# Performance work log

Measured on AMD Instinct MI355X. Metric: run time of the kernel, lower is better.

Reference implementation:

```python
import jax, jax.numpy as jnp
import numpy as np
import math

D_MODEL = 512
N_HEADS = 8
WINDOW = 32
B, L, S = 4, 2048, 2048


def setup_inputs() -> dict:
    key = jax.random.key(0)
    ks = jax.random.split(key, 12)
    scale = 1.0 / math.sqrt(D_MODEL)
    inp = {
        "queries": jax.random.normal(ks[0], (B, L, D_MODEL), jnp.float32),
        "keys": jax.random.normal(ks[1], (B, S, D_MODEL), jnp.float32),
        "values": jax.random.normal(ks[2], (B, S, D_MODEL), jnp.float32),
        # TriangularCausalMask: True above the diagonal => masked
        "attn_mask": jnp.triu(jnp.ones((L, S), jnp.bool_), k=1)[None, None],
        "Wq": jax.random.normal(ks[3], (D_MODEL, D_MODEL), jnp.float32) * scale,
        "bq": jnp.zeros((D_MODEL,), jnp.float32),
        "Wk": jax.random.normal(ks[4], (D_MODEL, D_MODEL), jnp.float32) * scale,
        "bk": jnp.zeros((D_MODEL,), jnp.float32),
        "Wv": jax.random.normal(ks[5], (D_MODEL, D_MODEL), jnp.float32) * scale,
        "bv": jnp.zeros((D_MODEL,), jnp.float32),
        "Wo": jax.random.normal(ks[6], (D_MODEL, D_MODEL), jnp.float32) * scale,
        "bo": jnp.zeros((D_MODEL,), jnp.float32),
        "gamma": jnp.ones((1,), jnp.float32) * 0.5,
    }
    return inp


def reference(queries, keys, values, attn_mask, Wq, bq, Wk, bk, Wv, bv, Wo, bo, gamma):
    Bq, Lq, _ = queries.shape
    Sq = keys.shape[1]
    H = N_HEADS
    q = (queries @ Wq + bq).reshape(Bq, Lq, H, -1)  # [B,L,H,dk]
    k = (keys @ Wk + bk).reshape(Bq, Sq, H, -1)
    v = (values @ Wv + bv).reshape(Bq, Sq, H, -1)

    scores = jnp.einsum('blhd,bshd->bhls', q, k) / math.sqrt(D_MODEL)  # [B,H,L,S]

    # exponential decay on relative position
    rel = jnp.arange(Lq)[:, None] - jnp.arange(Sq)[None, :]  # [L,S]
    decay = jnp.exp(-gamma[0] * jnp.abs(rel).astype(scores.dtype))
    scores = scores * decay[None, None]

    # sliding-window mask (exact replica of _create_window_mask)
    t = jnp.arange(Lq)
    start = jnp.clip(t - WINDOW // 2, 0, None)
    end = jnp.clip(t + WINDOW // 2 + 1, None, Sq)
    wmask = (t[:, None] >= start[None, :]) & (t[:, None] < end[None, :])  # [L,S]
    neg_inf = jnp.asarray(-jnp.inf, scores.dtype)
    scores = jnp.where(wmask[None, None], scores, neg_inf)

    # causal mask: True = masked
    scores = jnp.where(attn_mask, neg_inf, scores)

    attn = jax.nn.softmax(scores, axis=-1)  # dropout is identity at eval
    context = jnp.einsum('bhls,bshd->blhd', attn, v).reshape(Bq, Lq, -1)
    out = context @ Wo + bo
    return (out, attn)
```

## Files before the change

kernel.cpp:

```cpp
#include <hip/hip_runtime.h>
#include <hip/hip_bf16.h>
#include <cstdint>
#include <cstddef>

#define D_MODEL 512
#define N_HEADS 8
#define HDIM 64
#define SEQ 2048
#define B_SZ 4
#define M_TOT (B_SZ * SEQ)
#define ATTN_ROWS (B_SZ * N_HEADS * SEQ)
#define PROJ_ELEMS ((size_t)M_TOT * D_MODEL)

typedef __bf16 bf16x8 __attribute__((ext_vector_type(8)));
typedef float  f32x4  __attribute__((ext_vector_type(4)));

__device__ __forceinline__ unsigned short f2bf(float x) {
    __bf16 b = (__bf16)x;
    return __builtin_bit_cast(unsigned short, b);
}
__device__ __forceinline__ float bf2f(unsigned short u) {
    __bf16 b = __builtin_bit_cast(__bf16, u);
    return (float)b;
}

__global__ __launch_bounds__(256) void fill_zero(float4* __restrict__ p, size_t n4) {
    size_t i = (size_t)blockIdx.x * blockDim.x + threadIdx.x;
    size_t stride = (size_t)gridDim.x * blockDim.x;
    float4 z; z.x = 0.f; z.y = 0.f; z.z = 0.f; z.w = 0.f;
    for (; i < n4; i += stride) p[i] = z;
}

struct CvtArgs {
    const float* src[3];
    unsigned short* dst[3];
};

__global__ __launch_bounds__(256) void cvt_k(CvtArgs ca) {
    const int z = blockIdx.z;
    const size_t i = ((size_t)blockIdx.x * 256 + threadIdx.x) * 8;
    const float* src = ca.src[z];
    float4 a = *(const float4*)&src[i];
    float4 b = *(const float4*)&src[i + 4];
    unsigned short outv[8];
    outv[0] = f2bf(a.x); outv[1] = f2bf(a.y); outv[2] = f2bf(a.z); outv[3] = f2bf(a.w);
    outv[4] = f2bf(b.x); outv[5] = f2bf(b.y); outv[6] = f2bf(b.z); outv[7] = f2bf(b.w);
    *(uint4*)&ca.dst[z][i] = *(const uint4*)outv;
}

struct TransArgs {
    const float* W[4];
    unsigned short* Wt[4];
};

__global__ void transpose_k(TransArgs ta) {
    __shared__ float tile[32][33];
    const int z = blockIdx.z;
    const float* W = ta.W[z];
    unsigned short* Wt = ta.Wt[z];
    int x = blockIdx.x * 32 + threadIdx.x;
    int y0 = blockIdx.y * 32;
    for (int j = threadIdx.y; j < 32; j += 8)
        tile[j][threadIdx.x] = W[(size_t)(y0 + j) * D_MODEL + x];
    __syncthreads();
    int xo = blockIdx.y * 32 + threadIdx.x;
    int yo0 = blockIdx.x * 32;
    for (int j = threadIdx.y; j < 32; j += 8)
        Wt[(size_t)(yo0 + j) * D_MODEL + xo] = f2bf(tile[threadIdx.x][j]);
}

struct GemmArgs {
    const unsigned short* A[3];
    const unsigned short* Wt[3];
    const float* bias[3];
    void* C[3];
};

#define LDSTRIDE 72

template <int F32OUT>
__global__ __launch_bounds__(256, 2) void gemm_bt(GemmArgs ga) {
    __shared__ __align__(16) unsigned short lsA[128 * LDSTRIDE];
    __shared__ __align__(16) unsigned short lsB[128 * LDSTRIDE];

    const int z = blockIdx.z;
    const unsigned short* __restrict__ A  = ga.A[z];
    const unsigned short* __restrict__ Wt = ga.Wt[z];
    const float* __restrict__ bias        = ga.bias[z];

    const int m0 = blockIdx.x * 128;
    const int n0 = blockIdx.y * 128;
    const int tid = threadIdx.x;
    const int lane = tid & 63;
    const int wid = tid >> 6;
    const int wm = (wid >> 1) * 64;
    const int wn = (wid & 1) * 64;
    const int lrow = lane & 15;
    const int quad = lane >> 4;

    f32x4 acc[4][4];
#pragma unroll
    for (int i = 0; i < 4; ++i)
#pragma unroll
        for (int j = 0; j < 4; ++j)
            acc[i][j] = (f32x4){0.f, 0.f, 0.f, 0.f};

    for (int kt = 0; kt < D_MODEL; kt += 64) {
        __syncthreads();
#pragma unroll
        for (int p = 0; p < 4; ++p) {
            int c = p * 256 + tid;
            int r = c >> 3;
            int col = (c & 7) << 3;
            *(uint4*)&lsA[r * LDSTRIDE + col] =
                *(const uint4*)&A[(size_t)(m0 + r) * D_MODEL + kt + col];
        }
#pragma unroll
        for (int p = 0; p < 4; ++p) {
            int c = p * 256 + tid;
            int r = c >> 3;
            int col = (c & 7) << 3;
            *(uint4*)&lsB[r * LDSTRIDE + col] =
                *(const uint4*)&Wt[(size_t)(n0 + r) * D_MODEL + kt + col];
        }
        __syncthreads();
#pragma unroll
        for (int ks = 0; ks < 2; ++ks) {
            const int ko = ks * 32 + quad * 8;
            bf16x8 af[4], bfr[4];
#pragma unroll
            for (int mt = 0; mt < 4; ++mt)
                af[mt] = *(const bf16x8*)&lsA[(wm + mt * 16 + lrow) * LDSTRIDE + ko];
#pragma unroll
            for (int nt = 0; nt < 4; ++nt)
                bfr[nt] = *(const bf16x8*)&lsB[(wn + nt * 16 + lrow) * LDSTRIDE + ko];
#pragma unroll
            for (int mt = 0; mt < 4; ++mt)
#pragma unroll
                for (int nt = 0; nt < 4; ++nt)
                    acc[mt][nt] = __builtin_amdgcn_mfma_f32_16x16x32_bf16(
                        af[mt], bfr[nt], acc[mt][nt], 0, 0, 0);
        }
    }

#pragma unroll
    for (int nt = 0; nt < 4; ++nt) {
        const int gcol = n0 + wn + nt * 16 + lrow;
        const float bv = bias[gcol];
#pragma unroll
        for (int mt = 0; mt < 4; ++mt) {
            const int grow = m0 + wm + mt * 16 + quad * 4;
#pragma unroll
            for (int r = 0; r < 4; ++r) {
                const float v = acc[mt][nt][r] + bv;
                if (F32OUT)
                    ((float*)ga.C[z])[(size_t)(grow + r) * D_MODEL + gcol] = v;
                else
                    ((unsigned short*)ga.C[z])[(size_t)(grow + r) * D_MODEL + gcol] = f2bf(v);
            }
        }
    }
}

__global__ __launch_bounds__(256, 4) void attn_k(
    const unsigned short* __restrict__ Q,
    const unsigned short* __restrict__ K,
    const unsigned short* __restrict__ V,
    const float* __restrict__ gamma_p,
    float* __restrict__ attn_out,
    unsigned short* __restrict__ ctx) {
    const int wid = threadIdx.x >> 6;
    const int lane = threadIdx.x & 63;
    const int idx = blockIdx.x * 4 + wid;
    const int t = idx & (SEQ - 1);
    const int bh = idx >> 11;
    const int h = bh & (N_HEADS - 1);
    const int b = bh >> 3;

    const float g = gamma_p[0];
    int s0 = t - 16;
    if (s0 < 0) s0 = 0;
    const int cnt = t - s0 + 1;

    const size_t qrow = (size_t)b * SEQ + t;
    const int qcol = h * HDIM + lane;
    const float q = bf2f(Q[qrow * D_MODEL + qcol]);
    const float rs = 0.044194173824159216f;
    const size_t krowbase = (size_t)b * SEQ;

    float myscore = -__builtin_inff();
    float m = -__builtin_inff();
    for (int j = 0; j < cnt; ++j) {
        const int s = s0 + j;
        const float kv = bf2f(K[(krowbase + s) * D_MODEL + qcol]);
        float part = q * kv;
#pragma unroll
        for (int off = 32; off > 0; off >>= 1)
            part += __shfl_xor(part, off, 64);
        const float score = part * rs * __expf(-g * (float)(t - s));
        if (lane == j) myscore = score;
        m = fmaxf(m, score);
    }

    const float p = (lane < cnt) ? __expf(myscore - m) : 0.f;
    float l = p;
#pragma unroll
    for (int off = 32; off > 0; off >>= 1)
        l += __shfl_xor(l, off, 64);
    const float inv = 1.f / l;

    if (lane < cnt)
        attn_out[(size_t)idx * SEQ + s0 + lane] = p * inv;

    float acc = 0.f;
    for (int j = 0; j < cnt; ++j) {
        const float pj = __shfl(p, j, 64) * inv;
        const float vv = bf2f(V[(krowbase + s0 + j) * D_MODEL + qcol]);
        acc = fmaf(pj, vv, acc);
    }
    ctx[qrow * D_MODEL + qcol] = f2bf(acc);
}

extern "C" void kernel_launch(void* const* d_in, const int* in_sizes, int n_in,
                              void* d_out, int out_size, void* d_ws, size_t ws_size,
                              hipStream_t stream) {
    const float* queries = (const float*)d_in[0];
    const float* keys    = (const float*)d_in[1];
    const float* values  = (const float*)d_in[2];
    const float* Wq = (const float*)d_in[4];
    const float* bq = (const float*)d_in[5];
    const float* Wk = (const float*)d_in[6];
    const float* bk = (const float*)d_in[7];
    const float* Wv = (const float*)d_in[8];
    const float* bv = (const float*)d_in[9];
    const float* Wo = (const float*)d_in[10];
    const float* bo = (const float*)d_in[11];
    const float* gamma = (const float*)d_in[12];

    char* ws = (char*)d_ws;
    unsigned short* Qin = (unsigned short*)ws;
    unsigned short* Kin = Qin + PROJ_ELEMS;
    unsigned short* Vin = Kin + PROJ_ELEMS;
    unsigned short* WT  = Vin + PROJ_ELEMS;
    unsigned short* WqT = WT;
    unsigned short* WkT = WT + 262144;
    unsigned short* WvT = WT + 2 * 262144;
    unsigned short* WoT = WT + 3 * 262144;
    unsigned short* Qp  = WT + 4 * 262144;
    unsigned short* Kp  = Qp + PROJ_ELEMS;
    unsigned short* Vp  = Kp + PROJ_ELEMS;
    unsigned short* Ctx = Vp + PROJ_ELEMS;

    float* out_p  = (float*)d_out;
    float* attn_p = out_p + PROJ_ELEMS;

    const size_t n4 = (size_t)ATTN_ROWS * SEQ / 4;
    fill_zero<<<8192, 256, 0, stream>>>((float4*)attn_p, n4);

    CvtArgs ca;
    ca.src[0] = queries; ca.src[1] = keys; ca.src[2] = values;
    ca.dst[0] = Qin;     ca.dst[1] = Kin;  ca.dst[2] = Vin;
    cvt_k<<<dim3(PROJ_ELEMS / (256 * 8), 1, 3), 256, 0, stream>>>(ca);

    TransArgs ta;
    ta.W[0] = Wq;  ta.W[1] = Wk;  ta.W[2] = Wv;  ta.W[3] = Wo;
    ta.Wt[0] = WqT; ta.Wt[1] = WkT; ta.Wt[2] = WvT; ta.Wt[3] = WoT;
    transpose_k<<<dim3(16, 16, 4), dim3(32, 8), 0, stream>>>(ta);

    GemmArgs gq;
    gq.A[0] = Qin;   gq.A[1] = Kin;  gq.A[2] = Vin;
    gq.Wt[0] = WqT;  gq.Wt[1] = WkT; gq.Wt[2] = WvT;
    gq.bias[0] = bq; gq.bias[1] = bk; gq.bias[2] = bv;
    gq.C[0] = Qp;    gq.C[1] = Kp;   gq.C[2] = Vp;
    gemm_bt<0><<<dim3(M_TOT / 128, D_MODEL / 128, 3), 256, 0, stream>>>(gq);

    attn_k<<<ATTN_ROWS / 4, 256, 0, stream>>>(Qp, Kp, Vp, gamma, attn_p, Ctx);

    GemmArgs go;
    go.A[0] = Ctx;   go.Wt[0] = WoT; go.bias[0] = bo; go.C[0] = out_p;
    go.A[1] = Ctx;   go.Wt[1] = WoT; go.bias[1] = bo; go.C[1] = out_p;
    go.A[2] = Ctx;   go.Wt[2] = WoT; go.bias[2] = bo; go.C[2] = out_p;
    gemm_bt<1><<<dim3(M_TOT / 128, D_MODEL / 128, 1), 256, 0, stream>>>(go);
}
```

Before: 766.9 us.

## Tile sliding-window attention with LDS-staged K/V and 4 lanes per query row

Replaces the one-wavefront-per-row attention kernel with a block that handles 64 query rows of one head. The block stages the shared K/V window rows in LDS, and each row is computed by 4 lanes holding 16 dims each. This removes the long serial per-key loop of 64-lane shuffle reductions and the redundant global K/V reads. In exchange it adds LDS usage and register pressure, and makes the attention-probability stores strided across lanes.

```diff
diff --git a/kernel.cpp b/kernel.cpp
--- a/kernel.cpp
+++ b/kernel.cpp
@@ -162,63 +162,107 @@
     }
 }
 
-__global__ __launch_bounds__(256, 4) void attn_k(
+#define KV_ROWS 80
+#define LROW 72
+
+__device__ __forceinline__ void load16f(const unsigned short* p, float* out) {
+    bf16x8 a = *(const bf16x8*)p;
+    bf16x8 b = *(const bf16x8*)(p + 8);
+#pragma unroll
+    for (int i = 0; i < 8; ++i) { out[i] = (float)a[i]; out[8 + i] = (float)b[i]; }
+}
+
+__global__ __launch_bounds__(256, 4) void attn2_k(
     const unsigned short* __restrict__ Q,
     const unsigned short* __restrict__ K,
     const unsigned short* __restrict__ V,
     const float* __restrict__ gamma_p,
     float* __restrict__ attn_out,
     unsigned short* __restrict__ ctx) {
-    const int wid = threadIdx.x >> 6;
-    const int lane = threadIdx.x & 63;
-    const int idx = blockIdx.x * 4 + wid;
-    const int t = idx & (SEQ - 1);
-    const int bh = idx >> 11;
-    const int h = bh & (N_HEADS - 1);
+    __shared__ __align__(16) unsigned short lk[KV_ROWS * LROW];
+    __shared__ __align__(16) unsigned short lv[KV_ROWS * LROW];
+
+    const int bh = blockIdx.y;
+    const int t0 = blockIdx.x * 64;
     const int b = bh >> 3;
+    const int h = bh & 7;
+    const int tid = threadIdx.x;
+    const int w = tid >> 6;
+    const int lane = tid & 63;
+    const int r = lane >> 2;
+    const int c = lane & 3;
 
     const float g = gamma_p[0];
-    int s0 = t - 16;
-    if (s0 < 0) s0 = 0;
-    const int cnt = t - s0 + 1;
-
-    const size_t qrow = (size_t)b * SEQ + t;
-    const int qcol = h * HDIM + lane;
-    const float q = bf2f(Q[qrow * D_MODEL + qcol]);
     const float rs = 0.044194173824159216f;
-    const size_t krowbase = (size_t)b * SEQ;
-
-    float myscore = -__builtin_inff();
-    float m = -__builtin_inff();
-    for (int j = 0; j < cnt; ++j) {
-        const int s = s0 + j;
-        const float kv = bf2f(K[(krowbase + s) * D_MODEL + qcol]);
-        float part = q * kv;
-#pragma unroll
-        for (int off = 32; off > 0; off >>= 1)
-            part += __shfl_xor(part, off, 64);
-        const float score = part * rs * __expf(-g * (float)(t - s));
-        if (lane == j) myscore = score;
-        m = fmaxf(m, score);
-    }
-
-    const float p = (lane < cnt) ? __expf(myscore - m) : 0.f;
-    float l = p;
-#pragma unroll
-    for (int off = 32; off > 0; off >>= 1)
-        l += __shfl_xor(l, off, 64);
+
+    const size_t srcbase = (size_t)b * SEQ * D_MODEL + (size_t)h * HDIM;
+    for (int idx = tid; idx < KV_ROWS * 8; idx += 256) {
+        const int row = idx >> 3;
+        const int ch = (idx & 7) * 8;
+        const int grow = t0 - 16 + row;
+        uint4 kv4 = {0, 0, 0, 0};
+        uint4 vv4 = {0, 0, 0, 0};
+        if (grow >= 0) {
+            const size_t off = srcbase + (size_t)grow * D_MODEL + ch;
+            kv4 = *(const uint4*)&K[off];
+            vv4 = *(const uint4*)&V[off];
+        }
+        *(uint4*)&lk[row * LROW + ch] = kv4;
+        *(uint4*)&lv[row * LROW + ch] = vv4;
+    }
+    __syncthreads();
+
+    const int gr = t0 + w * 16 + r;
+    const size_t qoff = srcbase + (size_t)gr * D_MODEL + c * 16;
+    float qv[16];
+    load16f(&Q[qoff], qv);
+
+    const int lr0 = w * 16 + r;
+    float scr[17];
+#pragma unroll
+    for (int j = 0; j < 17; ++j) {
+        float kvv[16];
+        load16f(&lk[(lr0 + j) * LROW + c * 16], kvv);
+        float part = 0.f;
+#pragma unroll
+        for (int i = 0; i < 16; ++i) part = fmaf(qv[i], kvv[i], part);
+        part += __shfl_xor(part, 1, 64);
+        part += __shfl_xor(part, 2, 64);
+        const float dec = __expf(-g * (float)(16 - j));
+        scr[j] = part * rs * dec;
+        if (gr - 16 + j < 0) scr[j] = -__builtin_inff();
+    }
+
+    float m = scr[0];
+#pragma unroll
+    for (int j = 1; j < 17; ++j) m = fmaxf(m, scr[j]);
+    float l = 0.f;
+#pragma unroll
+    for (int j = 0; j < 17; ++j) { scr[j] = __expf(scr[j] - m); l += scr[j]; }
     const float inv = 1.f / l;
 
-    if (lane < cnt)
-        attn_out[(size_t)idx * SEQ + s0 + lane] = p * inv;
-
-    float acc = 0.f;
-    for (int j = 0; j < cnt; ++j) {
-        const float pj = __shfl(p, j, 64) * inv;
-        const float vv = bf2f(V[(krowbase + s0 + j) * D_MODEL + qcol]);
-        acc = fmaf(pj, vv, acc);
-    }
-    ctx[qrow * D_MODEL + qcol] = f2bf(acc);
+    float acc[16];
+#pragma unroll
+    for (int i = 0; i < 16; ++i) acc[i] = 0.f;
+#pragma unroll
+    for (int j = 0; j < 17; ++j) {
+        float vv[16];
+        load16f(&lv[(lr0 + j) * LROW + c * 16], vv);
+#pragma unroll
+        for (int i = 0; i < 16; ++i) acc[i] = fmaf(scr[j], vv[i], acc[i]);
+    }
+
+    unsigned short outv[16];
+#pragma unroll
+    for (int i = 0; i < 16; ++i) outv[i] = f2bf(acc[i] * inv);
+    *(uint4*)&ctx[qoff]     = *(const uint4*)&outv[0];
+    *(uint4*)&ctx[qoff + 8] = *(const uint4*)&outv[8];
+
+    const size_t arow = ((size_t)bh * SEQ + gr) * SEQ;
+    for (int j = c; j < 17; j += 4) {
+        const int s = gr - 16 + j;
+        if (s >= 0) attn_out[arow + s] = scr[j] * inv;
+    }
 }
 
 extern "C" void kernel_launch(void* const* d_in, const int* in_sizes, int n_in,
@@ -274,7 +318,8 @@
     gq.C[0] = Qp;    gq.C[1] = Kp;   gq.C[2] = Vp;
     gemm_bt<0><<<dim3(M_TOT / 128, D_MODEL / 128, 3), 256, 0, stream>>>(gq);
 
-    attn_k<<<ATTN_ROWS / 4, 256, 0, stream>>>(Qp, Kp, Vp, gamma, attn_p, Ctx);
+    attn2_k<<<dim3(SEQ / 64, B_SZ * N_HEADS), 256, 0, stream>>>(
+        Qp, Kp, Vp, gamma, attn_p, Ctx);
 
     GemmArgs go;
     go.A[0] = Ctx;   go.Wt[0] = WoT; go.bias[0] = bo; go.C[0] = out_p;
```

New measurement: 706.3 us. -7.9%, faster.
